# Performance work log

Measured on AMD Instinct MI355X. Metric: run time of the kernel, lower is better.

Reference implementation:

```python
import jax, jax.numpy as jnp
import numpy as np

KH = KW = 3
PAD = 1

def _bilinear(img, ys, xs):
    # img: [B,C,H,W]; ys, xs: [B,K2,H,W] float sample coords (zero padding outside)
    B, C, H, W = img.shape
    y0 = jnp.floor(ys)
    x0 = jnp.floor(xs)
    wy = ys - y0  # frac weights
    wx = xs - x0
    b = jnp.arange(B)[:, None, None, None]

    def gather(yi, xi):
        valid = (yi >= 0) & (yi <= H - 1) & (xi >= 0) & (xi <= W - 1)
        yc = jnp.clip(yi, 0, H - 1).astype(jnp.int32)
        xc = jnp.clip(xi, 0, W - 1).astype(jnp.int32)
        v = img[b, :, yc, xc]  # [B,K2,H,W,C]
        return v * valid[..., None].astype(img.dtype)

    v00 = gather(y0, x0)
    v01 = gather(y0, x0 + 1)
    v10 = gather(y0 + 1, x0)
    v11 = gather(y0 + 1, x0 + 1)
    wy = wy[..., None]
    wx = wx[..., None]
    return ((1 - wy) * (1 - wx) * v00 + (1 - wy) * wx * v01
            + wy * (1 - wx) * v10 + wy * wx * v11)


def _deform_conv(x, offset, weight, bias):
    # torchvision deform_conv2d v1, stride=1, pad=1, dilation=1
    B, C, H, W = x.shape
    O = weight.shape[0]
    K2 = KH * KW
    off = offset.reshape(B, K2, 2, H, W)
    dy, dx = off[:, :, 0], off[:, :, 1]
    ki, kj = jnp.meshgrid(jnp.arange(KH), jnp.arange(KW), indexing='ij')
    ki = ki.reshape(K2).astype(x.dtype)
    kj = kj.reshape(K2).astype(x.dtype)
    hh = jnp.arange(H, dtype=x.dtype)
    ww = jnp.arange(W, dtype=x.dtype)
    ys = hh[None, None, :, None] - PAD + ki[None, :, None, None] + dy
    xs = ww[None, None, None, :] - PAD + kj[None, :, None, None] + dx
    sampled = _bilinear(x, ys, xs)  # [B,K2,H,W,C]
    out = jnp.einsum('bkhwc,ock->bohw', sampled, weight.reshape(O, C, K2))
    return out + bias[None, :, None, None]


def setup_inputs() -> dict:
    key = jax.random.key(0)
    ks = jax.random.split(key, 8)
    B, C, O, H, W = 8, 256, 256, 56, 56
    red = C // 16
    x = jax.random.normal(ks[0], (B, C, H, W), dtype=jnp.float32)
    w_off = jax.random.normal(ks[1], (2 * KH * KW, C, KH, KW), dtype=jnp.float32) * 0.005
    b_off = jax.random.normal(ks[2], (2 * KH * KW,), dtype=jnp.float32) * 0.01
    w_conv = jax.random.normal(ks[3], (O, C, KH, KW), dtype=jnp.float32) * (1.0 / np.sqrt(C * KH * KW))
    b_conv = jax.random.normal(ks[4], (O,), dtype=jnp.float32) * 0.01
    fc1 = jax.random.normal(ks[5], (red, C), dtype=jnp.float32) * (1.0 / np.sqrt(C))
    fc2 = jax.random.normal(ks[6], (C, red), dtype=jnp.float32) * (1.0 / np.sqrt(red))
    return {"x": x, "w_off": w_off, "b_off": b_off, "w_conv": w_conv,
            "b_conv": b_conv, "fc1": fc1, "fc2": fc2}


def reference(x, w_off, b_off, w_conv, b_conv, fc1, fc2):
    # SE gate
    y = jnp.mean(x, axis=(2, 3))                       # [B,C]
    h = jax.nn.relu(y @ fc1.T)                          # [B,C/16]
    s = jax.nn.sigmoid(h @ fc2.T)                       # [B,C]
    xs = x * s[:, :, None, None]
    # offset conv (standard conv2d, pad=1)
    offset = jax.lax.conv_general_dilated(
        xs, w_off, window_strides=(1, 1), padding=[(PAD, PAD), (PAD, PAD)],
        dimension_numbers=('NCHW', 'OIHW', 'NCHW')) + b_off[None, :, None, None]
    out = _deform_conv(xs, offset, w_conv, b_conv)
    return jnp.tanh(out)
```

## Files before the change

kernel.cpp:

```cpp
#include <hip/hip_runtime.h>
#include <math.h>

typedef __attribute__((ext_vector_type(8))) short short8;
typedef __attribute__((ext_vector_type(8))) _Float16 h16x8;
typedef __attribute__((ext_vector_type(4))) float f32x4;

#define BB 8
#define CC 256
#define OO 256
#define HH 56
#define WW 56
#define HWH 3136
#define RED 16

__device__ inline unsigned short f2h(float f) {
    _Float16 h = (_Float16)f;
    return __builtin_bit_cast(unsigned short, h);
}
__device__ inline float h2f(unsigned short u) {
    return (float)__builtin_bit_cast(_Float16, u);
}
__device__ inline unsigned pkrtz(float lo, float hi) {
    return __builtin_bit_cast(unsigned, __builtin_amdgcn_cvt_pkrtz(lo, hi));
}
__device__ inline float fast_tanh(float x) {
    float e = __expf(2.0f * x);
    return 1.0f - 2.0f / (e + 1.0f);
}
__device__ inline void gl2lds16(const void* g, void* l) {
    __builtin_amdgcn_global_load_lds((const __attribute__((address_space(1))) unsigned int*)g,
                                     (__attribute__((address_space(3))) unsigned int*)l, 16, 0, 0);
}
__device__ inline unsigned pkmul_lo(unsigned a, unsigned b) {
    unsigned d;
    asm("v_pk_mul_f16 %0, %1, %2 op_sel:[0,0] op_sel_hi:[1,0]" : "=v"(d) : "v"(a), "v"(b));
    return d;
}
__device__ inline unsigned pkfma_hi(unsigned a, unsigned b, unsigned c) {
    unsigned d;
    asm("v_pk_fma_f16 %0, %1, %2, %3 op_sel:[0,1,0] op_sel_hi:[1,1,1]" : "=v"(d) : "v"(a), "v"(b), "v"(c));
    return d;
}
__device__ inline unsigned pkfma_lo(unsigned a, unsigned b, unsigned c) {
    unsigned d;
    asm("v_pk_fma_f16 %0, %1, %2, %3 op_sel:[0,0,0] op_sel_hi:[1,0,1]" : "=v"(d) : "v"(a), "v"(b), "v"(c));
    return d;
}
__device__ inline unsigned pkmul(unsigned a, unsigned b) {
    unsigned d;
    asm("v_pk_mul_f16 %0, %1, %2" : "=v"(d) : "v"(a), "v"(b));
    return d;
}
__device__ inline void blend16(uint4 q0, uint4 q1, uint4 q2, uint4 q3,
                               uint2 cw, uint4 sp, char* dst) {
    unsigned o0 = pkmul_lo(q0.x, cw.x); o0 = pkfma_hi(q1.x, cw.x, o0);
    o0 = pkfma_lo(q2.x, cw.y, o0); o0 = pkfma_hi(q3.x, cw.y, o0); o0 = pkmul(o0, sp.x);
    unsigned o1 = pkmul_lo(q0.y, cw.x); o1 = pkfma_hi(q1.y, cw.x, o1);
    o1 = pkfma_lo(q2.y, cw.y, o1); o1 = pkfma_hi(q3.y, cw.y, o1); o1 = pkmul(o1, sp.y);
    unsigned o2 = pkmul_lo(q0.z, cw.x); o2 = pkfma_hi(q1.z, cw.x, o2);
    o2 = pkfma_lo(q2.z, cw.y, o2); o2 = pkfma_hi(q3.z, cw.y, o2); o2 = pkmul(o2, sp.z);
    unsigned o3 = pkmul_lo(q0.w, cw.x); o3 = pkfma_hi(q1.w, cw.x, o3);
    o3 = pkfma_lo(q2.w, cw.y, o3); o3 = pkfma_hi(q3.w, cw.y, o3); o3 = pkmul(o3, sp.w);
    *(uint4*)dst = make_uint4(o0, o1, o2, o3);
}

__global__ __launch_bounds__(256) void prep_w(const float* __restrict__ w_conv, const float* __restrict__ w_off,
                                              unsigned short* __restrict__ wbf, unsigned short* __restrict__ wbo,
                                              float* __restrict__ y) {
    int blk = blockIdx.x;
    int tid = threadIdx.x;
    if (blk < 288) {
        int idx = blk * 256 + tid;
        int lane = idx & 63;
        int f = (idx >> 6) & 3;
        int og = (idx >> 8) & 7;
        int t = idx >> 11;
        int kk = t >> 2, cc = t & 3;
        int n = f >> 1, kh = f & 1;
        int o = og * 32 + n * 16 + (lane & 15);
        int cb2 = cc * 64 + kh * 32 + ((lane >> 4) << 3);
        short8 r;
        #pragma unroll
        for (int e = 0; e < 8; ++e) r[e] = (short)f2h(w_conv[(size_t)(o * 256 + cb2 + e) * 9 + kk]);
        *(short8*)(wbf + (size_t)idx * 8) = r;
    } else if (blk < 324) {
        int idx = (blk - 288) * 256 + tid;
        int g = idx & 7;
        int o = (idx >> 3) & 31;
        int t = idx >> 8;
        int kk = t >> 2, cc = t & 3;
        int dst = (((o * 128 + g * 16) ^ ((o & 7) << 4)) >> 1);
        short8 r;
        #pragma unroll
        for (int e = 0; e < 8; ++e) {
            int c = cc * 64 + g * 8 + e;
            r[e] = (o < 18) ? (short)f2h(w_off[(size_t)(o * 256 + c) * 9 + kk]) : (short)0;
        }
        *(short8*)(wbo + (size_t)t * 2048 + dst) = r;
    } else {
        #pragma unroll
        for (int i = 0; i < 8; ++i) y[i * 256 + tid] = 0.f;
    }
}

__global__ __launch_bounds__(256) void prep_xt(const float* __restrict__ x, unsigned short* __restrict__ x_t,
                                               float* __restrict__ y) {
    __shared__ float t[64][65];
    int blk = blockIdx.x;
    int ct = blk & 3;
    int hwt = (blk >> 2) % 49;
    int b = blk / (4 * 49);
    int c0 = ct * 64, hw0 = hwt * 64;
    int tid = threadIdx.x;
    const float* xb = x + ((size_t)(b * CC + c0)) * HWH + hw0;
    #pragma unroll
    for (int it = 0; it < 16; ++it) {
        int idx = it * 256 + tid;
        int c = idx >> 6, px = idx & 63;
        t[c][px] = xb[(size_t)c * HWH + px];
    }
    __syncthreads();
    unsigned short* xo = x_t + ((size_t)(b * HWH + hw0)) * CC + c0;
    #pragma unroll
    for (int it = 0; it < 16; ++it) {
        int idx = it * 256 + tid;
        int px = idx >> 6, c = idx & 63;
        xo[(size_t)px * CC + c] = f2h(t[c][px]);
    }
    int c = tid >> 2, seg = tid & 3;
    float sum = 0.f;
    #pragma unroll
    for (int i = 0; i < 16; ++i) sum += t[c][seg * 16 + i];
    sum += __shfl_down(sum, 1);
    sum += __shfl_down(sum, 2);
    if (seg == 0) atomicAdd(&y[b * 256 + c0 + c], sum);
}

__global__ __launch_bounds__(256) void se_fc(const float* __restrict__ y, const float* __restrict__ fc1,
                                             const float* __restrict__ fc2, float* __restrict__ s) {
    __shared__ float hbuf[BB * RED];
    const float inv = 1.0f / HWH;
    int t = threadIdx.x;
    if (t < BB * RED) {
        int b = t / RED, r = t % RED;
        float acc = 0.f;
        for (int c = 0; c < CC; ++c) acc += (y[b * CC + c] * inv) * fc1[r * CC + c];
        hbuf[t] = fmaxf(acc, 0.f);
    }
    __syncthreads();
    for (int i = t; i < BB * CC; i += 256) {
        int b = i / CC, c = i % CC;
        float acc = 0.f;
        #pragma unroll
        for (int r = 0; r < RED; ++r) acc += hbuf[b * RED + r] * fc2[c * RED + r];
        s[i] = 1.0f / (1.0f + expf(-acc));
    }
}

__global__ __launch_bounds__(256) void offset_mfma(const unsigned short* __restrict__ x_t,
                                                   const float* __restrict__ s,
                                                   const unsigned short* __restrict__ wbo,
                                                   const float* __restrict__ b_off,
                                                   int4* __restrict__ ci, uint2* __restrict__ cfh) {
    __shared__ __align__(16) char As[4][4096];
    __shared__ __align__(16) char Bs[4][4096];
    __shared__ float red[128 * 8];
    __shared__ float obuf[18 * 32];
    __shared__ float s_lds[256];
    int blk = blockIdx.x;
    blk = (blk & 7) * 98 + (blk >> 3);
    int b = blk / 98;
    int hw0 = (blk % 98) * 32;
    int tid = threadIdx.x;
    int lane = tid & 63, wv = tid >> 6;
    int ks = wv >> 1, m = wv & 1;
    int r0 = lane & 15, kb = (lane >> 4) << 4;
    int px = tid >> 3, c8 = tid & 7;
    int hwp = hw0 + px;
    int hp = hwp / 56, wp_ = hwp - hp * 56;
    int awoff = (px * 128 + c8 * 16) ^ ((px & 7) << 4);
    f32x4 zero = {0.f, 0.f, 0.f, 0.f};
    f32x4 acc[2] = {zero, zero};

    s_lds[tid] = s[b * 256 + tid];
    __syncthreads();

    auto buildA = [&](int q, int r, int buf) {
        int t = q * 18 + r;
        int kk = t >> 2, cc = t & 3;
        int hh = hp + kk / 3 - 1, ww = wp_ + kk % 3 - 1;
        short8 v = {0, 0, 0, 0, 0, 0, 0, 0};
        if (hh >= 0 && hh < 56 && ww >= 0 && ww < 56)
            v = *(const short8*)(x_t + (((size_t)(b * HWH + hh * 56 + ww)) << 8) + cc * 64 + c8 * 8);
        const float* sp_ = &s_lds[cc * 64 + c8 * 8];
        unsigned p0 = pkrtz(h2f((unsigned short)v[0]) * sp_[0], h2f((unsigned short)v[1]) * sp_[1]);
        unsigned p1 = pkrtz(h2f((unsigned short)v[2]) * sp_[2], h2f((unsigned short)v[3]) * sp_[3]);
        unsigned p2 = pkrtz(h2f((unsigned short)v[4]) * sp_[4], h2f((unsigned short)v[5]) * sp_[5]);
        unsigned p3 = pkrtz(h2f((unsigned short)v[6]) * sp_[6], h2f((unsigned short)v[7]) * sp_[7]);
        *(uint4*)(As[q * 2 + buf] + awoff) = make_uint4(p0, p1, p2, p3);
    };
    auto stageB = [&](int q, int r, int buf) {
        int t = q * 18 + r;
        gl2lds16(wbo + (size_t)t * 2048 + tid * 8, Bs[q * 2 + buf] + (tid >> 6) * 1024);
    };

    stageB(0, 0, 0); stageB(1, 0, 0);
    buildA(0, 0, 0); buildA(1, 0, 0);
    __syncthreads();

    #pragma unroll 2
    for (int r = 0; r < 18; ++r) {
        int cur = r & 1;
        if (r < 17) {
            stageB(0, r + 1, cur ^ 1); stageB(1, r + 1, cur ^ 1);
            buildA(0, r + 1, cur ^ 1); buildA(1, r + 1, cur ^ 1);
        }
        h16x8 a[2];
        #pragma unroll
        for (int kh = 0; kh < 2; ++kh) {
            int row = m * 16 + r0;
            int ao = (row * 128 + kh * 64 + kb) ^ ((row & 7) << 4);
            a[kh] = __builtin_bit_cast(h16x8, *(const short8*)(As[ks * 2 + cur] + ao));
        }
        #pragma unroll
        for (int n = 0; n < 2; ++n)
            #pragma unroll
            for (int kh = 0; kh < 2; ++kh) {
                int brow = n * 16 + r0;
                int bo = (brow * 128 + kh * 64 + kb) ^ ((brow & 7) << 4);
                h16x8 bv = __builtin_bit_cast(h16x8, *(const short8*)(Bs[ks * 2 + cur] + bo));
                acc[n] = __builtin_amdgcn_mfma_f32_16x16x32_f16(a[kh], bv, acc[n], 0, 0, 0);
            }
        __syncthreads();
    }

    if (ks == 1) {
        #pragma unroll
        for (int n = 0; n < 2; ++n)
            *(f32x4*)&red[(m * 64 + lane) * 8 + n * 4] = acc[n];
    }
    __syncthreads();
    if (ks == 0) {
        #pragma unroll
        for (int n = 0; n < 2; ++n) {
            f32x4 o2 = *(const f32x4*)&red[(m * 64 + lane) * 8 + n * 4];
            acc[n] += o2;
            int o = n * 16 + r0;
            if (o < 18) {
                float bia = b_off[o];
                #pragma unroll
                for (int j = 0; j < 4; ++j)
                    obuf[o * 32 + m * 16 + ((lane >> 4) << 2) + j] = acc[n][j] + bia;
            }
        }
    }
    __syncthreads();
    for (int i = tid; i < 288; i += 256) {
        int pxi = i & 31, kk = i >> 5;
        int hw = hw0 + pxi;
        int h = hw / 56, w = hw - h * 56;
        float dy = obuf[(kk * 2) * 32 + pxi];
        float dx = obuf[(kk * 2 + 1) * 32 + pxi];
        float ys = (float)(h - 1 + kk / 3) + dy;
        float xs = (float)(w - 1 + kk % 3) + dx;
        float y0f = floorf(ys), x0f = floorf(xs);
        float wy = ys - y0f, wx = xs - x0f;
        int y0 = (int)y0f, x0 = (int)x0f;
        int bi[4]; float wt[4];
        #pragma unroll
        for (int j = 0; j < 4; ++j) {
            int yj = y0 + (j >> 1), xj = x0 + (j & 1);
            bool val = yj >= 0 && yj < 56 && xj >= 0 && xj < 56;
            int yc = min(max(yj, 0), 55), xc = min(max(xj, 0), 55);
            wt[j] = val ? ((j >> 1) ? wy : 1.f - wy) * ((j & 1) ? wx : 1.f - wx) : 0.f;
            bi[j] = (b * HWH + yc * 56 + xc) << 8;
        }
        int idx = (b * 9 + kk) * HWH + hw;
        ci[idx] = make_int4(bi[0], bi[1], bi[2], bi[3]);
        cfh[idx] = make_uint2(pkrtz(wt[0], wt[1]), pkrtz(wt[2], wt[3]));
    }
}

__global__ __launch_bounds__(512) void deform_mfma(const unsigned short* __restrict__ x_t,
                                                   const float* __restrict__ s,
                                                   const int4* __restrict__ ci,
                                                   const uint2* __restrict__ cfh,
                                                   const unsigned short* __restrict__ wbf,
                                                   const float* __restrict__ b_conv,
                                                   float* __restrict__ out) {
    __shared__ __align__(16) char As[32768];
    int blk = blockIdx.x;
    blk = (blk & 7) * 49 + (blk >> 3);
    int b = blk / 49;
    int hw0 = (blk % 49) * 64;
    int tid = threadIdx.x;
    int lane = tid & 63, og = tid >> 6;
    int px = tid >> 3, cg = tid & 7;
    int r0 = lane & 15, kb = (lane >> 4) << 4;
    int awoff = px * 128 + (cg * 16 ^ ((px & 7) << 4));
    int cidx0 = b * 9 * HWH + hw0 + px;
    const unsigned short* wbB = wbf + og * 2048 + lane * 8;

    uint4 sp4[4];
    #pragma unroll
    for (int cc = 0; cc < 4; ++cc) {
        float4 s0 = *(const float4*)(s + b * 256 + cc * 64 + cg * 8);
        float4 s1 = *(const float4*)(s + b * 256 + cc * 64 + cg * 8 + 4);
        sp4[cc] = make_uint4(pkrtz(s0.x, s0.y), pkrtz(s0.z, s0.w), pkrtz(s1.x, s1.y), pkrtz(s1.z, s1.w));
    }

    f32x4 zero = {0.f, 0.f, 0.f, 0.f};
    f32x4 acc[4][2];
    #pragma unroll
    for (int m = 0; m < 4; ++m)
        #pragma unroll
        for (int n = 0; n < 2; ++n) acc[m][n] = zero;

    int4 cbL = ci[cidx0];
    uint2 cwB = cfh[cidx0];
    int4 cbN = ci[cidx0 + HWH];
    uint2 cwM = cfh[cidx0 + HWH];
    uint2 cwP = cwM;

    uint4 crn0[4], crn1[4];
    short8 bv[4];
    const unsigned short* wbK = wbB + 16384;

    {
        uint4 q[4];
        int c00 = cg * 8;
        q[0] = *(const uint4*)(x_t + cbL.x + c00);
        q[1] = *(const uint4*)(x_t + cbL.y + c00);
        q[2] = *(const uint4*)(x_t + cbL.z + c00);
        q[3] = *(const uint4*)(x_t + cbL.w + c00);
        int c02 = 128 + cg * 8;
        crn0[0] = *(const uint4*)(x_t + cbL.x + c02);
        crn0[1] = *(const uint4*)(x_t + cbL.y + c02);
        crn0[2] = *(const uint4*)(x_t + cbL.z + c02);
        crn0[3] = *(const uint4*)(x_t + cbL.w + c02);
        int c03 = 192 + cg * 8;
        crn1[0] = *(const uint4*)(x_t + cbL.x + c03);
        crn1[1] = *(const uint4*)(x_t + cbL.y + c03);
        crn1[2] = *(const uint4*)(x_t + cbL.z + c03);
        crn1[3] = *(const uint4*)(x_t + cbL.w + c03);
        #pragma unroll
        for (int f = 0; f < 4; ++f) bv[f] = *(const short8*)(wbB + f * 512);
        blend16(q[0], q[1], q[2], q[3], cwB, sp4[0], As + awoff);
        int c01 = 64 + cg * 8;
        q[0] = *(const uint4*)(x_t + cbL.x + c01);
        q[1] = *(const uint4*)(x_t + cbL.y + c01);
        q[2] = *(const uint4*)(x_t + cbL.z + c01);
        q[3] = *(const uint4*)(x_t + cbL.w + c01);
        blend16(q[0], q[1], q[2], q[3], cwB, sp4[1], As + 8192 + awoff);
    }
    __syncthreads();

#define PHASE(CCV, CRN) { \
    constexpr int CCc = (CCV); \
    if (CCc == 0) cbL = cbN; \
    h16x8 a_[4][2]; \
    { constexpr int tb_ = CCc * 8192; \
      _Pragma("unroll") for (int m_ = 0; m_ < 4; ++m_) \
      _Pragma("unroll") for (int kh_ = 0; kh_ < 2; ++kh_) { \
        int row_ = m_ * 16 + r0; \
        int ao_ = row_ * 128 + ((kh_ * 64 + kb) ^ ((row_ & 7) << 4)); \
        a_[m_][kh_] = __builtin_bit_cast(h16x8, *(const short8*)(As + tb_ + ao_)); } } \
    __builtin_amdgcn_s_setprio(1); \
    _Pragma("unroll") for (int n_ = 0; n_ < 2; ++n_) \
      _Pragma("unroll") for (int kh_ = 0; kh_ < 2; ++kh_) \
        _Pragma("unroll") for (int m_ = 0; m_ < 4; ++m_) \
          acc[m_][n_] = __builtin_amdgcn_mfma_f32_16x16x32_f16(a_[m_][kh_], __builtin_bit_cast(h16x8, bv[n_ * 2 + kh_]), acc[m_][n_], 0, 0, 0); \
    __builtin_amdgcn_s_setprio(0); \
    if (kk < 8 || CCc < 3) { \
        _Pragma("unroll") for (int f_ = 0; f_ < 4; ++f_) bv[f_] = *(const short8*)(wbK + f_ * 512); } \
    wbK += 16384; \
    if (CCc == 2) { cwB = cwM; cwM = cwP; } \
    if (kk < 8 || CCc < 2) { \
        blend16(CRN[0], CRN[1], CRN[2], CRN[3], cwB, sp4[(CCc + 2) & 3], \
                As + ((CCc + 2) & 3) * 8192 + awoff); } \
    if (kk < 8) { \
        constexpr int c0_ = CCc * 64; \
        CRN[0] = *(const uint4*)(x_t + cbL.x + c0_ + cg * 8); \
        CRN[1] = *(const uint4*)(x_t + cbL.y + c0_ + cg * 8); \
        CRN[2] = *(const uint4*)(x_t + cbL.z + c0_ + cg * 8); \
        CRN[3] = *(const uint4*)(x_t + cbL.w + c0_ + cg * 8); } \
    if (CCc == 1 && kk <= 6) { \
        int cidx = cidx0 + (kk + 2) * HWH; \
        cbN = ci[cidx]; cwP = cfh[cidx]; } \
    if (CCc & 1) __syncthreads(); }

    #pragma unroll 1
    for (int kk = 0; kk < 9; ++kk) {
        PHASE(0, crn0);
        PHASE(1, crn1);
        PHASE(2, crn0);
        PHASE(3, crn1);
    }
#undef PHASE

    #pragma unroll
    for (int n = 0; n < 2; ++n) {
        int o = og * 32 + n * 16 + r0;
        float bia = b_conv[o];
        #pragma unroll
        for (int m = 0; m < 4; ++m) {
            int pxo = hw0 + m * 16 + ((lane >> 4) << 2);
            float4 v;
            v.x = fast_tanh(acc[m][n][0] + bia);
            v.y = fast_tanh(acc[m][n][1] + bia);
            v.z = fast_tanh(acc[m][n][2] + bia);
            v.w = fast_tanh(acc[m][n][3] + bia);
            *(float4*)(out + ((size_t)(b * OO + o)) * HWH + pxo) = v;
        }
    }
}

extern "C" void kernel_launch(void* const* d_in, const int* in_sizes, int n_in,
                              void* d_out, int out_size, void* d_ws, size_t ws_size,
                              hipStream_t stream) {
    const float* x      = (const float*)d_in[0];
    const float* w_off  = (const float*)d_in[1];
    const float* b_off  = (const float*)d_in[2];
    const float* w_conv = (const float*)d_in[3];
    const float* b_conv = (const float*)d_in[4];
    const float* fc1    = (const float*)d_in[5];
    const float* fc2    = (const float*)d_in[6];
    float* out = (float*)d_out;
    float* ws  = (float*)d_ws;

    float* y = ws;
    float* s = y + 2048;
    unsigned short* x_t = (unsigned short*)(s + 2048);
    unsigned short* wbo = x_t + 6422528;
    unsigned short* wbf = wbo + 73728;
    int4*  ci  = (int4*)(wbf + 589824);
    uint2* cfh = (uint2*)(ci + 225792);

    prep_w<<<325, 256, 0, stream>>>(w_conv, w_off, wbf, wbo, y);
    prep_xt<<<BB * 49 * 4, 256, 0, stream>>>(x, x_t, y);
    se_fc<<<1, 256, 0, stream>>>(y, fc1, fc2, s);
    offset_mfma<<<BB * 98, 256, 0, stream>>>(x_t, s, wbo, b_off, ci, cfh);
    deform_mfma<<<BB * 49, 512, 0, stream>>>(x_t, s, ci, cfh, wbf, b_conv, out);
}
```

Measured before the change: 102.5 us.

## Merge weight prep into transpose kernel and inline SE gate into consumers

Folds the weight-repacking blocks into the x-transpose kernel as extra blocks, replaces the y-zeroing blocks with a memset, and drops the single-block se_fc kernel. Each offset and deform block now recomputes the SE gate for its batch from the pooled sums. This cuts two kernel launches and the serial one-block SE step. In exchange every block repeats the small FC work (a 16x256 and a 256x16 product), adds a barrier, and uses the less precise __expf.

```diff
diff --git a/kernel.cpp b/kernel.cpp
--- a/kernel.cpp
+++ b/kernel.cpp
@@ -64,54 +64,53 @@
     *(uint4*)dst = make_uint4(o0, o1, o2, o3);
 }
 
-__global__ __launch_bounds__(256) void prep_w(const float* __restrict__ w_conv, const float* __restrict__ w_off,
-                                              unsigned short* __restrict__ wbf, unsigned short* __restrict__ wbo,
-                                              float* __restrict__ y) {
+__global__ __launch_bounds__(256) void prep_xt(const float* __restrict__ x,
+                                               const float* __restrict__ w_conv,
+                                               const float* __restrict__ w_off,
+                                               unsigned short* __restrict__ x_t,
+                                               unsigned short* __restrict__ wbf,
+                                               unsigned short* __restrict__ wbo,
+                                               float* __restrict__ y) {
     int blk = blockIdx.x;
     int tid = threadIdx.x;
-    if (blk < 288) {
-        int idx = blk * 256 + tid;
-        int lane = idx & 63;
-        int f = (idx >> 6) & 3;
-        int og = (idx >> 8) & 7;
-        int t = idx >> 11;
-        int kk = t >> 2, cc = t & 3;
-        int n = f >> 1, kh = f & 1;
-        int o = og * 32 + n * 16 + (lane & 15);
-        int cb2 = cc * 64 + kh * 32 + ((lane >> 4) << 3);
-        short8 r;
-        #pragma unroll
-        for (int e = 0; e < 8; ++e) r[e] = (short)f2h(w_conv[(size_t)(o * 256 + cb2 + e) * 9 + kk]);
-        *(short8*)(wbf + (size_t)idx * 8) = r;
-    } else if (blk < 324) {
-        int idx = (blk - 288) * 256 + tid;
-        int g = idx & 7;
-        int o = (idx >> 3) & 31;
-        int t = idx >> 8;
-        int kk = t >> 2, cc = t & 3;
-        int dst = (((o * 128 + g * 16) ^ ((o & 7) << 4)) >> 1);
-        short8 r;
-        #pragma unroll
-        for (int e = 0; e < 8; ++e) {
-            int c = cc * 64 + g * 8 + e;
-            r[e] = (o < 18) ? (short)f2h(w_off[(size_t)(o * 256 + c) * 9 + kk]) : (short)0;
-        }
-        *(short8*)(wbo + (size_t)t * 2048 + dst) = r;
-    } else {
-        #pragma unroll
-        for (int i = 0; i < 8; ++i) y[i * 256 + tid] = 0.f;
-    }
-}
-
-__global__ __launch_bounds__(256) void prep_xt(const float* __restrict__ x, unsigned short* __restrict__ x_t,
-                                               float* __restrict__ y) {
+    if (blk >= 1568) {
+        int wb = blk - 1568;
+        if (wb < 288) {
+            int idx = wb * 256 + tid;
+            int lane = idx & 63;
+            int f = (idx >> 6) & 3;
+            int og = (idx >> 8) & 7;
+            int t = idx >> 11;
+            int kk = t >> 2, cc = t & 3;
+            int n = f >> 1, kh = f & 1;
+            int o = og * 32 + n * 16 + (lane & 15);
+            int cb2 = cc * 64 + kh * 32 + ((lane >> 4) << 3);
+            short8 r;
+            #pragma unroll
+            for (int e = 0; e < 8; ++e) r[e] = (short)f2h(w_conv[(size_t)(o * 256 + cb2 + e) * 9 + kk]);
+            *(short8*)(wbf + (size_t)idx * 8) = r;
+        } else {
+            int idx = (wb - 288) * 256 + tid;
+            int g = idx & 7;
+            int o = (idx >> 3) & 31;
+            int t = idx >> 8;
+            int kk = t >> 2, cc = t & 3;
+            int dst = (((o * 128 + g * 16) ^ ((o & 7) << 4)) >> 1);
+            short8 r;
+            #pragma unroll
+            for (int e = 0; e < 8; ++e) {
+                int c = cc * 64 + g * 8 + e;
+                r[e] = (o < 18) ? (short)f2h(w_off[(size_t)(o * 256 + c) * 9 + kk]) : (short)0;
+            }
+            *(short8*)(wbo + (size_t)t * 2048 + dst) = r;
+        }
+        return;
+    }
     __shared__ float t[64][65];
-    int blk = blockIdx.x;
     int ct = blk & 3;
     int hwt = (blk >> 2) % 49;
     int b = blk / (4 * 49);
     int c0 = ct * 64, hw0 = hwt * 64;
-    int tid = threadIdx.x;
     const float* xb = x + ((size_t)(b * CC + c0)) * HWH + hw0;
     #pragma unroll
     for (int it = 0; it < 16; ++it) {
@@ -136,29 +135,34 @@
     if (seg == 0) atomicAdd(&y[b * 256 + c0 + c], sum);
 }
 
-__global__ __launch_bounds__(256) void se_fc(const float* __restrict__ y, const float* __restrict__ fc1,
-                                             const float* __restrict__ fc2, float* __restrict__ s) {
-    __shared__ float hbuf[BB * RED];
-    const float inv = 1.0f / HWH;
-    int t = threadIdx.x;
-    if (t < BB * RED) {
-        int b = t / RED, r = t % RED;
+__device__ inline void se_inline(int tid, int b, const float* __restrict__ y,
+                                 const float* __restrict__ fc1, const float* __restrict__ fc2,
+                                 float* __restrict__ h_lds, float* __restrict__ s_out) {
+    if (tid < 256) {
+        int r = tid >> 4, cseg = tid & 15;
+        float part = 0.f;
+        #pragma unroll
+        for (int i = 0; i < 16; ++i)
+            part += y[b * 256 + cseg * 16 + i] * fc1[r * 256 + cseg * 16 + i];
+        part += __shfl_down(part, 8);
+        part += __shfl_down(part, 4);
+        part += __shfl_down(part, 2);
+        part += __shfl_down(part, 1);
+        if (cseg == 0) h_lds[r] = fmaxf(part * (1.0f / HWH), 0.f);
+    }
+    __syncthreads();
+    if (tid < 256) {
         float acc = 0.f;
-        for (int c = 0; c < CC; ++c) acc += (y[b * CC + c] * inv) * fc1[r * CC + c];
-        hbuf[t] = fmaxf(acc, 0.f);
-    }
-    __syncthreads();
-    for (int i = t; i < BB * CC; i += 256) {
-        int b = i / CC, c = i % CC;
-        float acc = 0.f;
-        #pragma unroll
-        for (int r = 0; r < RED; ++r) acc += hbuf[b * RED + r] * fc2[c * RED + r];
-        s[i] = 1.0f / (1.0f + expf(-acc));
+        #pragma unroll
+        for (int rr = 0; rr < 16; ++rr) acc += h_lds[rr] * fc2[tid * 16 + rr];
+        s_out[tid] = 1.0f / (1.0f + __expf(-acc));
     }
 }
 
 __global__ __launch_bounds__(256) void offset_mfma(const unsigned short* __restrict__ x_t,
-                                                   const float* __restrict__ s,
+                                                   const float* __restrict__ y,
+                                                   const float* __restrict__ fc1,
+                                                   const float* __restrict__ fc2,
                                                    const unsigned short* __restrict__ wbo,
                                                    const float* __restrict__ b_off,
                                                    int4* __restrict__ ci, uint2* __restrict__ cfh) {
@@ -167,6 +171,7 @@
     __shared__ float red[128 * 8];
     __shared__ float obuf[18 * 32];
     __shared__ float s_lds[256];
+    __shared__ float h_lds[16];
     int blk = blockIdx.x;
     blk = (blk & 7) * 98 + (blk >> 3);
     int b = blk / 98;
@@ -182,7 +187,7 @@
     f32x4 zero = {0.f, 0.f, 0.f, 0.f};
     f32x4 acc[2] = {zero, zero};
 
-    s_lds[tid] = s[b * 256 + tid];
+    se_inline(tid, b, y, fc1, fc2, h_lds, s_lds);
     __syncthreads();
 
     auto buildA = [&](int q, int r, int buf) {
@@ -282,13 +287,17 @@
 }
 
 __global__ __launch_bounds__(512) void deform_mfma(const unsigned short* __restrict__ x_t,
-                                                   const float* __restrict__ s,
+                                                   const float* __restrict__ y,
+                                                   const float* __restrict__ fc1,
+                                                   const float* __restrict__ fc2,
                                                    const int4* __restrict__ ci,
                                                    const uint2* __restrict__ cfh,
                                                    const unsigned short* __restrict__ wbf,
                                                    const float* __restrict__ b_conv,
                                                    float* __restrict__ out) {
     __shared__ __align__(16) char As[32768];
+    __shared__ __align__(16) float s_buf[256];
+    __shared__ float h_lds[16];
     int blk = blockIdx.x;
     blk = (blk & 7) * 49 + (blk >> 3);
     int b = blk / 49;
@@ -301,11 +310,14 @@
     int cidx0 = b * 9 * HWH + hw0 + px;
     const unsigned short* wbB = wbf + og * 2048 + lane * 8;
 
+    se_inline(tid, b, y, fc1, fc2, h_lds, s_buf);
+    __syncthreads();
+
     uint4 sp4[4];
     #pragma unroll
     for (int cc = 0; cc < 4; ++cc) {
-        float4 s0 = *(const float4*)(s + b * 256 + cc * 64 + cg * 8);
-        float4 s1 = *(const float4*)(s + b * 256 + cc * 64 + cg * 8 + 4);
+        float4 s0 = *(const float4*)&s_buf[cc * 64 + cg * 8];
+        float4 s1 = *(const float4*)&s_buf[cc * 64 + cg * 8 + 4];
         sp4[cc] = make_uint4(pkrtz(s0.x, s0.y), pkrtz(s0.z, s0.w), pkrtz(s1.x, s1.y), pkrtz(s1.z, s1.w));
     }
 
@@ -429,16 +441,14 @@
     float* ws  = (float*)d_ws;
 
     float* y = ws;
-    float* s = y + 2048;
-    unsigned short* x_t = (unsigned short*)(s + 2048);
+    unsigned short* x_t = (unsigned short*)(y + 2048);
     unsigned short* wbo = x_t + 6422528;
     unsigned short* wbf = wbo + 73728;
     int4*  ci  = (int4*)(wbf + 589824);
     uint2* cfh = (uint2*)(ci + 225792);
 
-    prep_w<<<325, 256, 0, stream>>>(w_conv, w_off, wbf, wbo, y);
-    prep_xt<<<BB * 49 * 4, 256, 0, stream>>>(x, x_t, y);
-    se_fc<<<1, 256, 0, stream>>>(y, fc1, fc2, s);
-    offset_mfma<<<BB * 98, 256, 0, stream>>>(x_t, s, wbo, b_off, ci, cfh);
-    deform_mfma<<<BB * 49, 512, 0, stream>>>(x_t, s, ci, cfh, wbf, b_conv, out);
-}
+    hipMemsetAsync(y, 0, 2048 * sizeof(float), stream);
+    prep_xt<<<1892, 256, 0, stream>>>(x, w_conv, w_off, x_t, wbf, wbo, y);
+    offset_mfma<<<BB * 98, 256, 0, stream>>>(x_t, y, fc1, fc2, wbo, b_off, ci, cfh);
+    deform_mfma<<<BB * 49, 512, 0, stream>>>(x_t, y, fc1, fc2, ci, cfh, wbf, b_conv, out);
+}
```

Result: faster. 99.13 us, median of 3 (-3.3%).
